# Kernel optimization log

Measured on AMD Instinct MI355X. Metric: run time of the kernel, lower is better.

Reference implementation:

```python
import jax, jax.numpy as jnp
import numpy as np

WS = 7
NUM_HEADS = 8


def setup_inputs() -> dict:
    key = jax.random.key(0)
    ks = jax.random.split(key, 5)
    B, H, W, C = 8, 112, 112, 256
    s = 1.0 / np.sqrt(C)
    return {
        "x": jax.random.normal(ks[0], (B, H * W, C), dtype=jnp.float32),
        "qkv_w": jax.random.normal(ks[1], (3 * C, C), dtype=jnp.float32) * s,
        "qkv_b": jax.random.normal(ks[2], (3 * C,), dtype=jnp.float32) * 0.02,
        "proj_w": jax.random.normal(ks[3], (C, C), dtype=jnp.float32) * s,
        "proj_b": jax.random.normal(ks[4], (C,), dtype=jnp.float32) * 0.02,
        "H": H,
        "W": W,
    }


def reference(x, qkv_w, qkv_b, proj_w, proj_b, H, W):
    B, N, C = x.shape
    ws, nh = WS, NUM_HEADS
    hd = C // nh
    scale = hd ** (-0.5)
    # pad H, W up to multiples of ws (no-op when already divisible)
    pad_b = (ws - H % ws) % ws
    pad_r = (ws - W % ws) % ws
    xi = x.reshape(B, H, W, C)
    xi = jnp.pad(xi, ((0, 0), (0, pad_b), (0, pad_r), (0, 0)))
    Hp, Wp = H + pad_b, W + pad_r
    _h, _w = Hp // ws, Wp // ws
    nwin = _h * _w
    # partition into windows: [B, nwin, ws*ws, C]
    xw = xi.reshape(B, _h, ws, _w, ws, C).transpose(0, 1, 3, 2, 4, 5)
    xw = xw.reshape(B, nwin, ws * ws, C)
    # qkv projection
    qkv = xw @ qkv_w.T + qkv_b  # [B, nwin, ws2, 3C]
    qkv = qkv.reshape(B, nwin, ws * ws, 3, nh, hd)
    q = qkv[..., 0, :, :].transpose(0, 1, 3, 2, 4)  # [B, nwin, nh, ws2, hd]
    k = qkv[..., 1, :, :].transpose(0, 1, 3, 2, 4)
    v = qkv[..., 2, :, :].transpose(0, 1, 3, 2, 4)
    attn = jnp.einsum('bwhqd,bwhkd->bwhqk', q, k) * scale
    attn = jax.nn.softmax(attn, axis=-1)
    o = jnp.einsum('bwhqk,bwhkd->bwhqd', attn, v)  # [B, nwin, nh, ws2, hd]
    o = o.transpose(0, 1, 3, 2, 4).reshape(B, _h, _w, ws, ws, C)
    o = o.transpose(0, 1, 3, 2, 4, 5).reshape(B, Hp, Wp, C)
    o = o[:, :H, :W, :].reshape(B, N, C)
    out = o @ proj_w.T + proj_b
    return out
```

## Files before the change

### kernel.cpp

```cpp
#include <hip/hip_runtime.h>
#include <cstdint>
#include <cstddef>


typedef __attribute__((ext_vector_type(8))) short bf16x8;
typedef __attribute__((ext_vector_type(4))) float f32x4;

#define MFMA_BF16(a, b, c) __builtin_amdgcn_mfma_f32_16x16x32_bf16((a), (b), (c), 0, 0, 0)

__device__ __forceinline__ unsigned short f2bf(float f) {
  unsigned int u = __builtin_bit_cast(unsigned int, f);
  u += 0x7fffu + ((u >> 16) & 1u);
  return (unsigned short)(u >> 16);
}
__device__ __forceinline__ unsigned int pack2(float a, float b) {
  return (unsigned int)f2bf(a) | ((unsigned int)f2bf(b) << 16);
}
__device__ __forceinline__ void gl16(const unsigned short* g, unsigned short* l) {
  __builtin_amdgcn_global_load_lds(
      (const __attribute__((address_space(1))) unsigned int*)g,
      (__attribute__((address_space(3))) unsigned int*)l, 16, 0, 0);
}

__global__ __launch_bounds__(256) void k_conv(const float* __restrict__ x,
                                              unsigned short* __restrict__ xb) {
  const int NU = 3211264;
  for (int u = blockIdx.x * 256 + threadIdx.x; u < NU; u += 2048 * 256) {
    const float4 a = *reinterpret_cast<const float4*>(x + (size_t)u * 8);
    const float4 b = *reinterpret_cast<const float4*>(x + (size_t)u * 8 + 4);
    uint4 p;
    p.x = pack2(a.x, a.y); p.y = pack2(a.z, a.w);
    p.z = pack2(b.x, b.y); p.w = pack2(b.z, b.w);
    *reinterpret_cast<uint4*>(xb + (size_t)u * 8) = p;
  }
}

__global__ __launch_bounds__(256, 4) void k_qkv(const unsigned short* __restrict__ xb,
                                                const float* __restrict__ w,
                                                const float* __restrict__ bias,
                                                unsigned short* __restrict__ qkv) {
  __shared__ __align__(16) char lds[34816];
  unsigned short* As = (unsigned short*)lds;
  unsigned short* Bs = (unsigned short*)(lds + 16384);

  const int id = blockIdx.x;
  const int wg = (id & 7) * 588 + (id >> 3);
  const int mt = wg / 6, nt = wg - mt * 6;
  const int m0 = mt * 128, n0 = nt * 128;

  const int t = threadIdx.x, lane = t & 63, wid = t >> 6;
  const int wr = (wid >> 1) * 64, wc = (wid & 1) * 64;
  const int l15 = lane & 15, l4 = lane >> 4;

  const int rA = t >> 2, cA = (t & 3) * 8;
  const int rB = t >> 1, khB = (t & 1) * 16;

  const unsigned short* gA0 = xb + (size_t)(m0 + rA) * 256 + cA;
  const unsigned short* gA1 = xb + (size_t)(m0 + 64 + rA) * 256 + cA;
  const float* gB = w + (size_t)(n0 + rB) * 256 + khB;

  f32x4 acc[4][4] = {};

  gl16(gA0, As + t * 8);
  gl16(gA1, As + 2048 + t * 8);
  {
    float4 b0 = *reinterpret_cast<const float4*>(gB);
    float4 b1 = *reinterpret_cast<const float4*>(gB + 4);
    uint4 p; p.x = pack2(b0.x, b0.y); p.y = pack2(b0.z, b0.w);
    p.z = pack2(b1.x, b1.y); p.w = pack2(b1.z, b1.w);
    *reinterpret_cast<uint4*>(Bs + rB * 32 + khB) = p;
    float4 b2 = *reinterpret_cast<const float4*>(gB + 8);
    float4 b3 = *reinterpret_cast<const float4*>(gB + 12);
    uint4 q; q.x = pack2(b2.x, b2.y); q.y = pack2(b2.z, b2.w);
    q.z = pack2(b3.x, b3.y); q.w = pack2(b3.z, b3.w);
    *reinterpret_cast<uint4*>(Bs + rB * 32 + khB + 8) = q;
  }
  __syncthreads();

  for (int ks = 0; ks < 8; ++ks) {
    const int cur = ks & 1;
    float4 b0, b1, b2, b3;
    if (ks < 7) {
      const int k0 = (ks + 1) * 32;
      gl16(gA0 + k0, As + (cur ^ 1) * 4096 + t * 8);
      gl16(gA1 + k0, As + (cur ^ 1) * 4096 + 2048 + t * 8);
      b0 = *reinterpret_cast<const float4*>(gB + k0);
      b1 = *reinterpret_cast<const float4*>(gB + k0 + 4);
      b2 = *reinterpret_cast<const float4*>(gB + k0 + 8);
      b3 = *reinterpret_cast<const float4*>(gB + k0 + 12);
    }
    const unsigned short* Ab = As + cur * 4096;
    const unsigned short* Bb = Bs + cur * 4096;
    bf16x8 af[4], bfr[4];
#pragma unroll
    for (int i = 0; i < 4; ++i) {
      af[i]  = *reinterpret_cast<const bf16x8*>(Ab + (wr + i * 16 + l15) * 32 + l4 * 8);
      bfr[i] = *reinterpret_cast<const bf16x8*>(Bb + (wc + i * 16 + l15) * 32 + l4 * 8);
    }
#pragma unroll
    for (int mi = 0; mi < 4; ++mi)
#pragma unroll
      for (int ni = 0; ni < 4; ++ni)
        acc[mi][ni] = MFMA_BF16(af[mi], bfr[ni], acc[mi][ni]);
    if (ks < 7) {
      unsigned short* Bn = Bs + (cur ^ 1) * 4096;
      uint4 p; p.x = pack2(b0.x, b0.y); p.y = pack2(b0.z, b0.w);
      p.z = pack2(b1.x, b1.y); p.w = pack2(b1.z, b1.w);
      *reinterpret_cast<uint4*>(Bn + rB * 32 + khB) = p;
      uint4 q; q.x = pack2(b2.x, b2.y); q.y = pack2(b2.z, b2.w);
      q.z = pack2(b3.x, b3.y); q.w = pack2(b3.z, b3.w);
      *reinterpret_cast<uint4*>(Bn + rB * 32 + khB + 8) = q;
    }
    __syncthreads();
  }

  float bv[4];
#pragma unroll
  for (int ni = 0; ni < 4; ++ni) bv[ni] = bias[n0 + wc + ni * 16 + l15];
  unsigned short* Cst = (unsigned short*)lds;
#pragma unroll
  for (int mi = 0; mi < 4; ++mi)
#pragma unroll
    for (int ni = 0; ni < 4; ++ni)
#pragma unroll
      for (int r = 0; r < 4; ++r)
        Cst[(wr + mi * 16 + l4 * 4 + r) * 136 + wc + ni * 16 + l15] =
            f2bf(acc[mi][ni][r] + bv[ni]);
  __syncthreads();

  const int which = n0 >> 8;
  const int hbase = (n0 >> 5) & 7;
#pragma unroll
  for (int p = 0; p < 2; ++p) {
    const int pair = p * 256 + t;
    const int token = pair & 127, hidx = pair >> 7;
    const int mrow = m0 + token;
    const int b = mrow / 12544, pix = mrow - b * 12544;
    const int py = pix / 112, px = pix - py * 112;
    const int wy = py / 7, ty = py - wy * 7;
    const int wxx = px / 7, tx = px - wxx * 7;
    const int win = wy * 16 + wxx, tloc = ty * 7 + tx;
    const unsigned short* src = Cst + token * 136 + hidx * 32;
    unsigned short* dst = qkv +
        (((size_t)(b * 256 + win) * 3 + which) * 8 + hbase + hidx) * 1568 + tloc * 32;
#pragma unroll
    for (int c = 0; c < 4; ++c)
      *reinterpret_cast<uint4*>(dst + c * 8) = *reinterpret_cast<const uint4*>(src + c * 8);
  }
}

__global__ __launch_bounds__(64) void k_attn(const unsigned short* __restrict__ qkv,
                                             unsigned short* __restrict__ o) {
  __shared__ unsigned short vT[32 * 64];
  __shared__ unsigned short Pl[64 * 64];

  const int lane = threadIdx.x;
  const int l15 = lane & 15, l4 = lane >> 4;

  const int bid = blockIdx.x;
  const int h = bid & 7;
  const int bw = bid >> 3;
  const int b = bw >> 8, win = bw & 255;

  const unsigned short* qg = qkv + ((size_t)bw * 24 + h) * 1568;
  const unsigned short* kg = qkv + ((size_t)bw * 24 + 8 + h) * 1568;
  const unsigned short* vg = qkv + ((size_t)bw * 24 + 16 + h) * 1568;

#pragma unroll
  for (int it = 0; it < 4; ++it) {
    const int j = it * 16 + (lane >> 2), d0 = (lane & 3) * 8;
    uint4 vv = {0, 0, 0, 0};
    if (j < 49) vv = *reinterpret_cast<const uint4*>(vg + j * 32 + d0);
    union { uint4 v; unsigned short u[8]; } un; un.v = vv;
#pragma unroll
    for (int e = 0; e < 8; ++e) {
      const int d = d0 + e;
      vT[d * 64 + ((((j >> 3) ^ (d & 7)) << 3) | (j & 7))] = un.u[e];
    }
  }

  f32x4 s[4][4] = {};
  {
    bf16x8 kf[4];
#pragma unroll
    for (int nj = 0; nj < 4; ++nj)
      kf[nj] = *reinterpret_cast<const bf16x8*>(kg + (nj * 16 + l15) * 32 + l4 * 8);
#pragma unroll
    for (int mi = 0; mi < 4; ++mi) {
      const bf16x8 qf = *reinterpret_cast<const bf16x8*>(qg + (mi * 16 + l15) * 32 + l4 * 8);
#pragma unroll
      for (int nj = 0; nj < 4; ++nj)
        s[mi][nj] = MFMA_BF16(qf, kf[nj], s[mi][nj]);
    }
  }

  const float scale = 0.17677669529663687f;
#pragma unroll
  for (int mi = 0; mi < 4; ++mi) {
#pragma unroll
    for (int r = 0; r < 4; ++r) {
      float v[4]; float mx = -3.0e38f;
#pragma unroll
      for (int nj = 0; nj < 4; ++nj) {
        const int col = nj * 16 + l15;
        float sv = s[mi][nj][r] * scale;
        sv = (col < 49) ? sv : -3.0e38f;
        v[nj] = sv; mx = fmaxf(mx, sv);
      }
#pragma unroll
      for (int off = 1; off < 16; off <<= 1) mx = fmaxf(mx, __shfl_xor(mx, off));
      float e[4]; float sum = 0.f;
#pragma unroll
      for (int nj = 0; nj < 4; ++nj) { e[nj] = __expf(v[nj] - mx); sum += e[nj]; }
#pragma unroll
      for (int off = 1; off < 16; off <<= 1) sum += __shfl_xor(sum, off);
      const float inv = 1.0f / sum;
      const int row = mi * 16 + l4 * 4 + r;
#pragma unroll
      for (int nj = 0; nj < 4; ++nj) {
        const int col = nj * 16 + l15;
        Pl[row * 64 + ((((col >> 3) ^ (row & 7)) << 3) | (col & 7))] = f2bf(e[nj] * inv);
      }
    }
  }

  f32x4 oa[4][2] = {};
#pragma unroll
  for (int ksj = 0; ksj < 2; ++ksj) {
    const int chunk = ksj * 4 + l4;
    bf16x8 vb[2];
#pragma unroll
    for (int dt = 0; dt < 2; ++dt) {
      const int d = dt * 16 + l15;
      vb[dt] = *reinterpret_cast<const bf16x8*>(&vT[d * 64 + ((chunk ^ (d & 7)) << 3)]);
    }
#pragma unroll
    for (int mi = 0; mi < 4; ++mi) {
      const int row = mi * 16 + l15;
      const bf16x8 pa = *reinterpret_cast<const bf16x8*>(&Pl[row * 64 + ((chunk ^ (row & 7)) << 3)]);
#pragma unroll
      for (int dt = 0; dt < 2; ++dt)
        oa[mi][dt] = MFMA_BF16(pa, vb[dt], oa[mi][dt]);
    }
  }

  asm volatile("s_waitcnt lgkmcnt(0)" ::: "memory");
  __builtin_amdgcn_sched_barrier(0);
  unsigned short* Ost = Pl;
#pragma unroll
  for (int mi = 0; mi < 4; ++mi)
#pragma unroll
    for (int r = 0; r < 4; ++r) {
      const int i = mi * 16 + l4 * 4 + r;
#pragma unroll
      for (int dt = 0; dt < 2; ++dt)
        Ost[i * 40 + dt * 16 + l15] = f2bf(oa[mi][dt][r]);
    }

  const int wy = win >> 4, wx = win & 15;
  if (lane < 49) {
    const int ty = lane / 7, tx = lane - ty * 7;
    const size_t m = (size_t)b * 12544 + (size_t)(wy * 7 + ty) * 112 + (wx * 7 + tx);
    unsigned short* dst = o + m * 256 + h * 32;
#pragma unroll
    for (int c = 0; c < 4; ++c)
      *reinterpret_cast<uint4*>(dst + c * 8) =
          *reinterpret_cast<const uint4*>(Ost + lane * 40 + c * 8);
  }
}

__global__ __launch_bounds__(256, 4) void k_proj(const unsigned short* __restrict__ a,
                                                 const float* __restrict__ w,
                                                 const float* __restrict__ bias,
                                                 float* __restrict__ out) {
  __shared__ __align__(16) char lds[32768];
  unsigned short* As = (unsigned short*)lds;
  unsigned short* Bs = (unsigned short*)(lds + 16384);

  const int id = blockIdx.x;
  const int wg = (id & 7) * 196 + (id >> 3);
  const int mt = wg >> 1, nt = wg & 1;
  const int m0 = mt * 128, n0 = nt * 128;

  const int t = threadIdx.x, lane = t & 63, wid = t >> 6;
  const int wr = (wid >> 1) * 64, wc = (wid & 1) * 64;
  const int l15 = lane & 15, l4 = lane >> 4;

  const int rA = t >> 2, cA = (t & 3) * 8;
  const int rB = t >> 1, khB = (t & 1) * 16;

  const unsigned short* gA0 = a + (size_t)(m0 + rA) * 256 + cA;
  const unsigned short* gA1 = a + (size_t)(m0 + 64 + rA) * 256 + cA;
  const float* gB = w + (size_t)(n0 + rB) * 256 + khB;

  f32x4 acc[4][4] = {};

  gl16(gA0, As + t * 8);
  gl16(gA1, As + 2048 + t * 8);
  {
    float4 b0 = *reinterpret_cast<const float4*>(gB);
    float4 b1 = *reinterpret_cast<const float4*>(gB + 4);
    uint4 p; p.x = pack2(b0.x, b0.y); p.y = pack2(b0.z, b0.w);
    p.z = pack2(b1.x, b1.y); p.w = pack2(b1.z, b1.w);
    *reinterpret_cast<uint4*>(Bs + rB * 32 + khB) = p;
    float4 b2 = *reinterpret_cast<const float4*>(gB + 8);
    float4 b3 = *reinterpret_cast<const float4*>(gB + 12);
    uint4 q; q.x = pack2(b2.x, b2.y); q.y = pack2(b2.z, b2.w);
    q.z = pack2(b3.x, b3.y); q.w = pack2(b3.z, b3.w);
    *reinterpret_cast<uint4*>(Bs + rB * 32 + khB + 8) = q;
  }
  __syncthreads();

  for (int ks = 0; ks < 8; ++ks) {
    const int cur = ks & 1;
    float4 b0, b1, b2, b3;
    if (ks < 7) {
      const int k0 = (ks + 1) * 32;
      gl16(gA0 + k0, As + (cur ^ 1) * 4096 + t * 8);
      gl16(gA1 + k0, As + (cur ^ 1) * 4096 + 2048 + t * 8);
      b0 = *reinterpret_cast<const float4*>(gB + k0);
      b1 = *reinterpret_cast<const float4*>(gB + k0 + 4);
      b2 = *reinterpret_cast<const float4*>(gB + k0 + 8);
      b3 = *reinterpret_cast<const float4*>(gB + k0 + 12);
    }
    const unsigned short* Ab = As + cur * 4096;
    const unsigned short* Bb = Bs + cur * 4096;
    bf16x8 af[4], bfr[4];
#pragma unroll
    for (int i = 0; i < 4; ++i) {
      af[i]  = *reinterpret_cast<const bf16x8*>(Ab + (wr + i * 16 + l15) * 32 + l4 * 8);
      bfr[i] = *reinterpret_cast<const bf16x8*>(Bb + (wc + i * 16 + l15) * 32 + l4 * 8);
    }
#pragma unroll
    for (int mi = 0; mi < 4; ++mi)
#pragma unroll
      for (int ni = 0; ni < 4; ++ni)
        acc[mi][ni] = MFMA_BF16(af[mi], bfr[ni], acc[mi][ni]);
    if (ks < 7) {
      unsigned short* Bn = Bs + (cur ^ 1) * 4096;
      uint4 p; p.x = pack2(b0.x, b0.y); p.y = pack2(b0.z, b0.w);
      p.z = pack2(b1.x, b1.y); p.w = pack2(b1.z, b1.w);
      *reinterpret_cast<uint4*>(Bn + rB * 32 + khB) = p;
      uint4 q; q.x = pack2(b2.x, b2.y); q.y = pack2(b2.z, b2.w);
      q.z = pack2(b3.x, b3.y); q.w = pack2(b3.z, b3.w);
      *reinterpret_cast<uint4*>(Bn + rB * 32 + khB + 8) = q;
    }
    __syncthreads();
  }

  float bv[4];
#pragma unroll
  for (int ni = 0; ni < 4; ++ni) bv[ni] = bias[n0 + wc + ni * 16 + l15];
#pragma unroll
  for (int mi = 0; mi < 4; ++mi)
#pragma unroll
    for (int r = 0; r < 4; ++r) {
      const int mrow = m0 + wr + mi * 16 + l4 * 4 + r;
      float* orow = out + (size_t)mrow * 256 + n0 + wc;
#pragma unroll
      for (int ni = 0; ni < 4; ++ni)
        orow[ni * 16 + l15] = acc[mi][ni][r] + bv[ni];
    }
}

extern "C" void kernel_launch(void* const* d_in, const int* in_sizes, int n_in,
                              void* d_out, int out_size, void* d_ws, size_t ws_size,
                              hipStream_t stream) {
  (void)in_sizes; (void)n_in; (void)out_size; (void)ws_size;
  const float* x      = (const float*)d_in[0];
  const float* qkv_w  = (const float*)d_in[1];
  const float* qkv_b  = (const float*)d_in[2];
  const float* proj_w = (const float*)d_in[3];
  const float* proj_b = (const float*)d_in[4];

  unsigned short* wsb  = (unsigned short*)d_ws;
  unsigned short* xb   = wsb;
  unsigned short* qkvg = wsb + 25690112;
  unsigned short* ob   = xb;
  float* out = (float*)d_out;

  k_conv<<<dim3(2048),  dim3(256), 0, stream>>>(x, xb);
  k_qkv <<<dim3(4704),  dim3(256), 0, stream>>>(xb, qkv_w, qkv_b, qkvg);
  k_attn<<<dim3(16384), dim3(64),  0, stream>>>(qkvg, ob);
  k_proj<<<dim3(1568),  dim3(256), 0, stream>>>(ob, proj_w, proj_b, out);
}
```

Measured before the change: 384.7 us.

## Pre-convert weights to bf16 and rebuild GEMM pipeline with swizzled async LDS loads

The conversion kernel now also converts the qkv and proj weights to bf16 once per call, into a workspace buffer. Both GEMM kernels then load A and B tiles directly into LDS with async global_load_lds, instead of converting fp32 weights in registers inside the K loop. The new main loop prefetches two stages ahead with explicit vmcnt waits and barriers, and uses an XOR swizzle on the LDS column slot to cut bank conflicts. The cost is an extra small conversion pass and more intricate manual synchronisation.

```diff
diff --git a/kernel.cpp b/kernel.cpp
--- a/kernel.cpp
+++ b/kernel.cpp
@@ -23,9 +23,12 @@
 }
 
 __global__ __launch_bounds__(256) void k_conv(const float* __restrict__ x,
-                                              unsigned short* __restrict__ xb) {
-  const int NU = 3211264;
-  for (int u = blockIdx.x * 256 + threadIdx.x; u < NU; u += 2048 * 256) {
+                                              unsigned short* __restrict__ xb,
+                                              const float* __restrict__ qkv_w,
+                                              const float* __restrict__ proj_w,
+                                              unsigned short* __restrict__ wbt) {
+  const int gid = blockIdx.x * 256 + threadIdx.x;
+  for (int u = gid; u < 3211264; u += 2048 * 256) {
     const float4 a = *reinterpret_cast<const float4*>(x + (size_t)u * 8);
     const float4 b = *reinterpret_cast<const float4*>(x + (size_t)u * 8 + 4);
     uint4 p;
@@ -33,10 +36,56 @@
     p.z = pack2(b.x, b.y); p.w = pack2(b.z, b.w);
     *reinterpret_cast<uint4*>(xb + (size_t)u * 8) = p;
   }
-}
+  if (gid < 32768) {
+    const float* s = (gid < 24576) ? qkv_w + (size_t)gid * 8
+                                   : proj_w + (size_t)(gid - 24576) * 8;
+    const float4 a = *reinterpret_cast<const float4*>(s);
+    const float4 b = *reinterpret_cast<const float4*>(s + 4);
+    uint4 p;
+    p.x = pack2(a.x, a.y); p.y = pack2(a.z, a.w);
+    p.z = pack2(b.x, b.y); p.w = pack2(b.z, b.w);
+    *reinterpret_cast<uint4*>(wbt + (size_t)gid * 8) = p;
+  }
+}
+
+#define GEMM_ISSUE(buf, kk)                                          \
+  do {                                                               \
+    gl16(gA + (kk) * 32,         As + (buf) * 4096 + t * 8);         \
+    gl16(gA + (kk) * 32 + 16384, As + (buf) * 4096 + 2048 + t * 8);  \
+    gl16(gB + (kk) * 32,         Bs + (buf) * 4096 + t * 8);         \
+    gl16(gB + (kk) * 32 + 16384, Bs + (buf) * 4096 + 2048 + t * 8);  \
+  } while (0)
+
+#define GEMM_MAIN_LOOP()                                                         \
+  GEMM_ISSUE(0, 0);                                                              \
+  GEMM_ISSUE(1, 1);                                                              \
+  for (int ks = 0; ks < 8; ++ks) {                                               \
+    const int cur = ks & 1;                                                      \
+    if (ks < 7) asm volatile("s_waitcnt vmcnt(4)" ::: "memory");                 \
+    else        asm volatile("s_waitcnt vmcnt(0)" ::: "memory");                 \
+    __builtin_amdgcn_s_barrier();                                                \
+    const unsigned short* Ab = As + cur * 4096;                                  \
+    const unsigned short* Bb = Bs + cur * 4096;                                  \
+    bf16x8 af[4], bfr[4];                                                        \
+    _Pragma("unroll") for (int i = 0; i < 4; ++i) {                              \
+      const int ra = wr + i * 16 + l15;                                          \
+      const int rb = wc + i * 16 + l15;                                          \
+      af[i]  = *reinterpret_cast<const bf16x8*>(                                 \
+          Ab + ra * 32 + ((l4 ^ ((ra >> 1) & 3)) * 8));                          \
+      bfr[i] = *reinterpret_cast<const bf16x8*>(                                 \
+          Bb + rb * 32 + ((l4 ^ ((rb >> 1) & 3)) * 8));                          \
+    }                                                                            \
+    asm volatile("s_waitcnt lgkmcnt(0)" ::: "memory");                           \
+    __builtin_amdgcn_sched_barrier(0);                                           \
+    __builtin_amdgcn_s_barrier();                                                \
+    if (ks < 6) GEMM_ISSUE(cur, ks + 2);                                         \
+    _Pragma("unroll") for (int mi = 0; mi < 4; ++mi)                             \
+      _Pragma("unroll") for (int ni = 0; ni < 4; ++ni)                           \
+        acc[mi][ni] = MFMA_BF16(af[mi], bfr[ni], acc[mi][ni]);                   \
+  }
 
 __global__ __launch_bounds__(256, 4) void k_qkv(const unsigned short* __restrict__ xb,
-                                                const float* __restrict__ w,
+                                                const unsigned short* __restrict__ wbq,
                                                 const float* __restrict__ bias,
                                                 unsigned short* __restrict__ qkv) {
   __shared__ __align__(16) char lds[34816];
@@ -52,71 +101,18 @@
   const int wr = (wid >> 1) * 64, wc = (wid & 1) * 64;
   const int l15 = lane & 15, l4 = lane >> 4;
 
-  const int rA = t >> 2, cA = (t & 3) * 8;
-  const int rB = t >> 1, khB = (t & 1) * 16;
-
-  const unsigned short* gA0 = xb + (size_t)(m0 + rA) * 256 + cA;
-  const unsigned short* gA1 = xb + (size_t)(m0 + 64 + rA) * 256 + cA;
-  const float* gB = w + (size_t)(n0 + rB) * 256 + khB;
+  float bv[4];
+#pragma unroll
+  for (int ni = 0; ni < 4; ++ni) bv[ni] = bias[n0 + wc + ni * 16 + l15];
+
+  const int row0 = t >> 2, slot = t & 3;
+  const int g = slot ^ ((row0 >> 1) & 3);
+  const unsigned short* gA = xb  + (size_t)(m0 + row0) * 256 + g * 8;
+  const unsigned short* gB = wbq + (size_t)(n0 + row0) * 256 + g * 8;
 
   f32x4 acc[4][4] = {};
-
-  gl16(gA0, As + t * 8);
-  gl16(gA1, As + 2048 + t * 8);
-  {
-    float4 b0 = *reinterpret_cast<const float4*>(gB);
-    float4 b1 = *reinterpret_cast<const float4*>(gB + 4);
-    uint4 p; p.x = pack2(b0.x, b0.y); p.y = pack2(b0.z, b0.w);
-    p.z = pack2(b1.x, b1.y); p.w = pack2(b1.z, b1.w);
-    *reinterpret_cast<uint4*>(Bs + rB * 32 + khB) = p;
-    float4 b2 = *reinterpret_cast<const float4*>(gB + 8);
-    float4 b3 = *reinterpret_cast<const float4*>(gB + 12);
-    uint4 q; q.x = pack2(b2.x, b2.y); q.y = pack2(b2.z, b2.w);
-    q.z = pack2(b3.x, b3.y); q.w = pack2(b3.z, b3.w);
-    *reinterpret_cast<uint4*>(Bs + rB * 32 + khB + 8) = q;
-  }
-  __syncthreads();
-
-  for (int ks = 0; ks < 8; ++ks) {
-    const int cur = ks & 1;
-    float4 b0, b1, b2, b3;
-    if (ks < 7) {
-      const int k0 = (ks + 1) * 32;
-      gl16(gA0 + k0, As + (cur ^ 1) * 4096 + t * 8);
-      gl16(gA1 + k0, As + (cur ^ 1) * 4096 + 2048 + t * 8);
-      b0 = *reinterpret_cast<const float4*>(gB + k0);
-      b1 = *reinterpret_cast<const float4*>(gB + k0 + 4);
-      b2 = *reinterpret_cast<const float4*>(gB + k0 + 8);
-      b3 = *reinterpret_cast<const float4*>(gB + k0 + 12);
-    }
-    const unsigned short* Ab = As + cur * 4096;
-    const unsigned short* Bb = Bs + cur * 4096;
-    bf16x8 af[4], bfr[4];
-#pragma unroll
-    for (int i = 0; i < 4; ++i) {
-      af[i]  = *reinterpret_cast<const bf16x8*>(Ab + (wr + i * 16 + l15) * 32 + l4 * 8);
-      bfr[i] = *reinterpret_cast<const bf16x8*>(Bb + (wc + i * 16 + l15) * 32 + l4 * 8);
-    }
-#pragma unroll
-    for (int mi = 0; mi < 4; ++mi)
-#pragma unroll
-      for (int ni = 0; ni < 4; ++ni)
-        acc[mi][ni] = MFMA_BF16(af[mi], bfr[ni], acc[mi][ni]);
-    if (ks < 7) {
-      unsigned short* Bn = Bs + (cur ^ 1) * 4096;
-      uint4 p; p.x = pack2(b0.x, b0.y); p.y = pack2(b0.z, b0.w);
-      p.z = pack2(b1.x, b1.y); p.w = pack2(b1.z, b1.w);
-      *reinterpret_cast<uint4*>(Bn + rB * 32 + khB) = p;
-      uint4 q; q.x = pack2(b2.x, b2.y); q.y = pack2(b2.z, b2.w);
-      q.z = pack2(b3.x, b3.y); q.w = pack2(b3.z, b3.w);
-      *reinterpret_cast<uint4*>(Bn + rB * 32 + khB + 8) = q;
-    }
-    __syncthreads();
-  }
-
-  float bv[4];
-#pragma unroll
-  for (int ni = 0; ni < 4; ++ni) bv[ni] = bias[n0 + wc + ni * 16 + l15];
+  GEMM_MAIN_LOOP();
+
   unsigned short* Cst = (unsigned short*)lds;
 #pragma unroll
   for (int mi = 0; mi < 4; ++mi)
@@ -270,7 +266,7 @@
 }
 
 __global__ __launch_bounds__(256, 4) void k_proj(const unsigned short* __restrict__ a,
-                                                 const float* __restrict__ w,
+                                                 const unsigned short* __restrict__ wbp,
                                                  const float* __restrict__ bias,
                                                  float* __restrict__ out) {
   __shared__ __align__(16) char lds[32768];
@@ -286,71 +282,18 @@
   const int wr = (wid >> 1) * 64, wc = (wid & 1) * 64;
   const int l15 = lane & 15, l4 = lane >> 4;
 
-  const int rA = t >> 2, cA = (t & 3) * 8;
-  const int rB = t >> 1, khB = (t & 1) * 16;
-
-  const unsigned short* gA0 = a + (size_t)(m0 + rA) * 256 + cA;
-  const unsigned short* gA1 = a + (size_t)(m0 + 64 + rA) * 256 + cA;
-  const float* gB = w + (size_t)(n0 + rB) * 256 + khB;
+  float bv[4];
+#pragma unroll
+  for (int ni = 0; ni < 4; ++ni) bv[ni] = bias[n0 + wc + ni * 16 + l15];
+
+  const int row0 = t >> 2, slot = t & 3;
+  const int g = slot ^ ((row0 >> 1) & 3);
+  const unsigned short* gA = a   + (size_t)(m0 + row0) * 256 + g * 8;
+  const unsigned short* gB = wbp + (size_t)(n0 + row0) * 256 + g * 8;
 
   f32x4 acc[4][4] = {};
-
-  gl16(gA0, As + t * 8);
-  gl16(gA1, As + 2048 + t * 8);
-  {
-    float4 b0 = *reinterpret_cast<const float4*>(gB);
-    float4 b1 = *reinterpret_cast<const float4*>(gB + 4);
-    uint4 p; p.x = pack2(b0.x, b0.y); p.y = pack2(b0.z, b0.w);
-    p.z = pack2(b1.x, b1.y); p.w = pack2(b1.z, b1.w);
-    *reinterpret_cast<uint4*>(Bs + rB * 32 + khB) = p;
-    float4 b2 = *reinterpret_cast<const float4*>(gB + 8);
-    float4 b3 = *reinterpret_cast<const float4*>(gB + 12);
-    uint4 q; q.x = pack2(b2.x, b2.y); q.y = pack2(b2.z, b2.w);
-    q.z = pack2(b3.x, b3.y); q.w = pack2(b3.z, b3.w);
-    *reinterpret_cast<uint4*>(Bs + rB * 32 + khB + 8) = q;
-  }
-  __syncthreads();
-
-  for (int ks = 0; ks < 8; ++ks) {
-    const int cur = ks & 1;
-    float4 b0, b1, b2, b3;
-    if (ks < 7) {
-      const int k0 = (ks + 1) * 32;
-      gl16(gA0 + k0, As + (cur ^ 1) * 4096 + t * 8);
-      gl16(gA1 + k0, As + (cur ^ 1) * 4096 + 2048 + t * 8);
-      b0 = *reinterpret_cast<const float4*>(gB + k0);
-      b1 = *reinterpret_cast<const float4*>(gB + k0 + 4);
-      b2 = *reinterpret_cast<const float4*>(gB + k0 + 8);
-      b3 = *reinterpret_cast<const float4*>(gB + k0 + 12);
-    }
-    const unsigned short* Ab = As + cur * 4096;
-    const unsigned short* Bb = Bs + cur * 4096;
-    bf16x8 af[4], bfr[4];
-#pragma unroll
-    for (int i = 0; i < 4; ++i) {
-      af[i]  = *reinterpret_cast<const bf16x8*>(Ab + (wr + i * 16 + l15) * 32 + l4 * 8);
-      bfr[i] = *reinterpret_cast<const bf16x8*>(Bb + (wc + i * 16 + l15) * 32 + l4 * 8);
-    }
-#pragma unroll
-    for (int mi = 0; mi < 4; ++mi)
-#pragma unroll
-      for (int ni = 0; ni < 4; ++ni)
-        acc[mi][ni] = MFMA_BF16(af[mi], bfr[ni], acc[mi][ni]);
-    if (ks < 7) {
-      unsigned short* Bn = Bs + (cur ^ 1) * 4096;
-      uint4 p; p.x = pack2(b0.x, b0.y); p.y = pack2(b0.z, b0.w);
-      p.z = pack2(b1.x, b1.y); p.w = pack2(b1.z, b1.w);
-      *reinterpret_cast<uint4*>(Bn + rB * 32 + khB) = p;
-      uint4 q; q.x = pack2(b2.x, b2.y); q.y = pack2(b2.z, b2.w);
-      q.z = pack2(b3.x, b3.y); q.w = pack2(b3.z, b3.w);
-      *reinterpret_cast<uint4*>(Bn + rB * 32 + khB + 8) = q;
-    }
-    __syncthreads();
-  }
-
-  float bv[4];
-#pragma unroll
-  for (int ni = 0; ni < 4; ++ni) bv[ni] = bias[n0 + wc + ni * 16 + l15];
+  GEMM_MAIN_LOOP();
+
 #pragma unroll
   for (int mi = 0; mi < 4; ++mi)
 #pragma unroll
@@ -376,11 +319,14 @@
   unsigned short* wsb  = (unsigned short*)d_ws;
   unsigned short* xb   = wsb;
   unsigned short* qkvg = wsb + 25690112;
+  unsigned short* wbt  = wsb + 102760448;
+  unsigned short* wbq  = wbt;
+  unsigned short* wbp  = wbt + 196608;
   unsigned short* ob   = xb;
   float* out = (float*)d_out;
 
-  k_conv<<<dim3(2048),  dim3(256), 0, stream>>>(x, xb);
-  k_qkv <<<dim3(4704),  dim3(256), 0, stream>>>(xb, qkv_w, qkv_b, qkvg);
+  k_conv<<<dim3(2048),  dim3(256), 0, stream>>>(x, xb, qkv_w, proj_w, wbt);
+  k_qkv <<<dim3(4704),  dim3(256), 0, stream>>>(xb, wbq, qkv_b, qkvg);
   k_attn<<<dim3(16384), dim3(64),  0, stream>>>(qkvg, ob);
-  k_proj<<<dim3(1568),  dim3(256), 0, stream>>>(ob, proj_w, proj_b, out);
-}
+  k_proj<<<dim3(1568),  dim3(256), 0, stream>>>(ob, wbp, proj_b, out);
+}
```

Result: faster. 357.8 us (-7.0%).
